# Kernel optimization log

Measured on AMD Instinct MI355X. Metric: run time of the kernel, lower is better.

## Reference

```python
import jax, jax.numpy as jnp
import numpy as np

B, C, H, W = 8, 128, 128, 128
NUM_HEADS = 4
KERNEL = 7
SH, SW = 16, 16


def setup_inputs() -> dict:
    key = jax.random.key(0)
    ks = jax.random.split(key, 5)
    s = 0.02
    return {
        "x": jax.random.normal(ks[0], (B, C, H, W), jnp.float32),
        "sims": jax.random.uniform(ks[1], (B, H, W, SH, SW), jnp.float32),
        "qk_w": jax.random.normal(ks[2], (2 * C, C), jnp.float32) * s,
        "v_w": jax.random.normal(ks[3], (C, C), jnp.float32) * s,
        "proj_w": jax.random.normal(ks[4], (C, C), jnp.float32) * s,
    }


def _nbr_starts(n, k):
    # NATTEN border handling: window start clamped so every query sees k neighbors
    return jnp.clip(jnp.arange(n) - k // 2, 0, n - k)


def reference(x, sims, qk_w, v_w, proj_w):
    Bb, Cc, Hh, Ww = x.shape
    hd = Cc // NUM_HEADS
    scale = hd ** -0.5
    xp = jnp.transpose(x, (0, 2, 3, 1))                       # [B,H,W,C]

    qk = xp @ qk_w.T                                           # [B,H,W,2C]
    q = (qk[..., :Cc]).reshape(Bb, Hh, Ww, NUM_HEADS, hd) * scale
    k = (qk[..., Cc:]).reshape(Bb, Hh, Ww, NUM_HEADS, hd)
    v = (xp @ v_w.T).reshape(Bb, Hh, Ww, NUM_HEADS, hd)

    sh_start = _nbr_starts(Hh, KERNEL)                         # [H]
    sw_start = _nbr_starts(Ww, KERNEL)                         # [W]

    # get_indices: nearest-interp superpixel grid label per pixel
    si = (jnp.arange(Hh) * SH) // Hh
    sj = (jnp.arange(Ww) * SW) // Ww
    slabel = si[:, None] * SW + sj[None, :]                    # [H,W]
    # hard superpixel assignment (argmax of sims); one_hot(argmax) gather
    # over sinds == equality test against the label map
    L = jnp.argmax(sims.reshape(Bb, Hh, Ww, SH * SW), axis=-1) # [B,H,W]

    attn_l, pi_l = [], []
    for di in range(KERNEL):
        hh = sh_start + di
        for dj in range(KERNEL):
            ww = sw_start + dj
            kk = k[:, hh][:, :, ww]                            # [B,H,W,h,d]
            attn_l.append(jnp.einsum('bijhd,bijhd->bhij', q, kk))
            pi_l.append((L[:, hh][:, :, ww] == slabel[None]).astype(x.dtype))
    attn = jnp.stack(attn_l, axis=-1)                          # [B,h,H,W,K2]
    pi = jnp.stack(pi_l, axis=-1)                              # [B,H,W,K2]

    # superpixel-masked softmax: softmax over window, reweight by membership
    # of neighbor in query's superpixel, renormalize
    p = jax.nn.softmax(attn, axis=-1) * pi[:, None]
    p = p / (jnp.sum(p, axis=-1, keepdims=True) + 1e-8)

    out = jnp.zeros_like(v)
    idx = 0
    for di in range(KERNEL):
        hh = sh_start + di
        for dj in range(KERNEL):
            ww = sw_start + dj
            vv = v[:, hh][:, :, ww]                            # [B,H,W,h,d]
            out = out + jnp.einsum('bhij,bijhd->bijhd', p[..., idx], vv)
            idx += 1

    out = out.reshape(Bb, Hh, Ww, Cc) @ proj_w.T               # proj
    return jnp.transpose(out, (0, 3, 1, 2))                    # [B,C,H,W]
```

## Files before the change

### kernel.cpp

```cpp
#include <hip/hip_runtime.h>
#include <hip/hip_bf16.h>

#define CCH 128
#define HHH 128
#define WWW 128
#define HWX 16384
#define NHD 4
#define HD  32
#define SCALE 0.17677669529663687f
#define LOG2E 1.4426950408889634f

typedef unsigned int  u32;
typedef unsigned short u16;
typedef short s16x8 __attribute__((ext_vector_type(8)));
typedef float f32x4 __attribute__((ext_vector_type(4)));

__device__ __forceinline__ u16 f2bf(float f) {
  u32 u = __float_as_uint(f);
  u += 0x7fffu + ((u >> 16) & 1u);
  return (u16)(u >> 16);
}
__device__ __forceinline__ u32 pk2(float a, float b) {
  return (u32)f2bf(a) | ((u32)f2bf(b) << 16);
}
__device__ __forceinline__ u32 pkru(float a, float b) {
  u32 ua = __float_as_uint(a) + 0x8000u;
  u32 ub = __float_as_uint(b) + 0x8000u;
  return __builtin_amdgcn_perm(ub, ua, 0x07060302);
}

__global__ __launch_bounds__(256) void wtrans_kernel(
    const float* __restrict__ qk_w, const float* __restrict__ v_w,
    const float* __restrict__ proj_w, u16* __restrict__ wfq, u16* __restrict__ wfp) {
  int idx = blockIdx.x * 256 + threadIdx.x;
  if (idx < 49152) {
    int j = idx & 7, l = (idx >> 3) & 63, kk = (idx >> 9) & 3, nt = idx >> 11;
    int k = kk * 32 + (l >> 4) * 8 + j;
    int oc = nt * 16 + (l & 15);
    float val;
    if (oc < 256) { val = qk_w[oc * 128 + k]; if (oc < 128) val *= SCALE * LOG2E; }
    else          { val = v_w[(oc - 256) * 128 + k]; }
    wfq[idx] = f2bf(val);
  } else {
    int r = idx - 49152;
    int j = r & 7, l = (r >> 3) & 63, kk = (r >> 9) & 3, mt = r >> 11;
    int oc = mt * 16 + (l & 15);
    int k = kk * 32 + (l >> 4) * 8 + j;
    wfp[r] = f2bf(proj_w[oc * 128 + k]);
  }
}

__global__ __launch_bounds__(256) void argmax_kernel(
    const float* __restrict__ sims, int* __restrict__ L) {
  const int wave = threadIdx.x >> 6, lane = threadIdx.x & 63;
  const int pix = blockIdx.x * 4 + wave;
  const float4 s4 = *(const float4*)(sims + (size_t)pix * 256 + lane * 4);
  float bv = s4.x; int bi = lane * 4;
  if (s4.y > bv) { bv = s4.y; bi = lane * 4 + 1; }
  if (s4.z > bv) { bv = s4.z; bi = lane * 4 + 2; }
  if (s4.w > bv) { bv = s4.w; bi = lane * 4 + 3; }
  #pragma unroll
  for (int off = 32; off > 0; off >>= 1) {
    float ov = __shfl_down(bv, off);
    int   oi = __shfl_down(bi, off);
    if (ov > bv || (ov == bv && oi < bi)) { bv = ov; bi = oi; }
  }
  if (lane == 0) L[pix] = bi;
}

__global__ __launch_bounds__(256) void qkv_kernel(
    const float* __restrict__ x, const u16* __restrict__ wfq,
    u16* __restrict__ qb, u16* __restrict__ kb, u16* __restrict__ vb) {
  __shared__ __align__(16) u16 xs[64 * 136];
  const int t = threadIdx.x;
  const int pg0 = blockIdx.x * 64;
  const int b = blockIdx.x >> 8;
  const int hw0 = pg0 & (HWX - 1);
  const float* xb = x + (size_t)b * (CCH * HWX) + hw0;
  u32* xsw = (u32*)xs;
  #pragma unroll
  for (int it = 0; it < 16; ++it) {
    int flat = t + it * 256;
    int pix = flat & 63, c2 = flat >> 6;
    float f0 = xb[(size_t)(2 * c2) * HWX + pix];
    float f1 = xb[(size_t)(2 * c2 + 1) * HWX + pix];
    xsw[pix * 68 + c2] = pk2(f0, f1);
  }
  __syncthreads();

  const int w = t >> 6, lane = t & 63;
  const int l15 = lane & 15, quad = lane >> 4;

  s16x8 af[4][4];
  #pragma unroll
  for (int m = 0; m < 4; ++m)
    #pragma unroll
    for (int kk = 0; kk < 4; ++kk)
      af[m][kk] = *(const s16x8*)(xs + (m * 16 + l15) * 136 + kk * 32 + quad * 8);

  f32x4 acc[6][4];
  #pragma unroll
  for (int nt = 0; nt < 6; ++nt)
    #pragma unroll
    for (int m = 0; m < 4; ++m) acc[nt][m] = (f32x4){0.f, 0.f, 0.f, 0.f};

  const u16* wl = wfq + lane * 8;
  #pragma unroll
  for (int nt = 0; nt < 6; ++nt) {
    const int ntg = w * 6 + nt;
    s16x8 bf[4];
    #pragma unroll
    for (int kk = 0; kk < 4; ++kk)
      bf[kk] = *(const s16x8*)(wl + (size_t)(ntg * 4 + kk) * 512);
    #pragma unroll
    for (int m = 0; m < 4; ++m)
      #pragma unroll
      for (int kk = 0; kk < 4; ++kk)
        acc[nt][m] = __builtin_amdgcn_mfma_f32_16x16x32_bf16(af[m][kk], bf[kk], acc[nt][m], 0, 0, 0);
  }

  #pragma unroll
  for (int nt = 0; nt < 6; ++nt) {
    const int oc = (w * 6 + nt) * 16 + l15;
    u16* base; int off;
    if (oc < 128)      { base = qb; off = oc; }
    else if (oc < 256) { base = kb; off = oc - 128; }
    else               { base = vb; off = oc - 256; }
    #pragma unroll
    for (int m = 0; m < 4; ++m) {
      const int pr = pg0 + m * 16 + quad * 4;
      #pragma unroll
      for (int r = 0; r < 4; ++r)
        base[((size_t)(pr + r) << 7) + off] = f2bf(acc[nt][m][r]);
    }
  }
}

#define VROW 520
#define PROW 72
__global__ __launch_bounds__(256, 2) void attn_kernel(
    const u16* __restrict__ qb, const u16* __restrict__ kb, const u16* __restrict__ vb,
    const int* __restrict__ L, u16* __restrict__ aob) {
  __shared__ __align__(16) u16 vT[32 * VROW];
  __shared__ __align__(16) u16 pT[256 * PROW];
  __shared__ __align__(16) u32 meta[512];
  const int t = threadIdx.x;
  const int bid = blockIdx.x;
  const int h = bid & 3, tj = (bid >> 2) & 7, ti = (bid >> 5) & 7, b = bid >> 8;
  const int i0 = ti * 16, j0 = tj * 16;
  const int r0 = i0 - 3, c0 = j0 - 3;
  const size_t bbase = (size_t)b * HWX;

  #pragma unroll
  for (int it = 0; it < 8; ++it) {
    int flat = t + it * 256;
    int key = flat >> 2, dq = flat & 3;
    int kr = key / 22, kc = key - kr * 22;
    int pr = min(max(r0 + kr, 0), HHH - 1), pc = min(max(c0 + kc, 0), WWW - 1);
    size_t g = ((bbase + (size_t)pr * WWW + pc) << 7) + h * HD + dq * 8;
    uint4 vv = *(const uint4*)(vb + g);
    u16* cb = vT + key + (size_t)(dq * 8) * VROW;
    cb[0 * VROW] = (u16)vv.x; cb[1 * VROW] = (u16)(vv.x >> 16);
    cb[2 * VROW] = (u16)vv.y; cb[3 * VROW] = (u16)(vv.y >> 16);
    cb[4 * VROW] = (u16)vv.z; cb[5 * VROW] = (u16)(vv.z >> 16);
    cb[6 * VROW] = (u16)vv.w; cb[7 * VROW] = (u16)(vv.w >> 16);
  }
  #pragma unroll
  for (int it = 0; it < 2; ++it) {
    int key = t + it * 256;
    int kr = key / 22, kc = key - kr * 22;
    int pr = min(max(r0 + kr, 0), HHH - 1), pc = min(max(c0 + kc, 0), WWW - 1);
    int lab = L[bbase + (size_t)pr * WWW + pc];
    u32 rm = 0;
    #pragma unroll
    for (int nt = 0; nt < 16; ++nt) {
      int rs = min(max(i0 + nt - 3, 0), HHH - 7) - r0;
      rm |= (u32)((u32)(kr - rs) <= 6u) << nt;
    }
    meta[key] = (u32)lab | ((u32)kc << 8) | (rm << 16);
  }
  __syncthreads();

  const int w = t >> 6, lane = t & 63;
  const int l15 = lane & 15, quad = lane >> 4;
  const int qj = j0 + l15;
  const u32 cs_rel = (u32)(min(max(qj - 3, 0), WWW - 7) - c0);
  const int ntg0 = w * 4;

  u32 slab[4];
  s16x8 qf[4];
  #pragma unroll
  for (int nt = 0; nt < 4; ++nt) {
    int qi = i0 + ntg0 + nt;
    slab[nt] = (u32)(((qi >> 3) << 4) | (qj >> 3));
    qf[nt] = *(const s16x8*)(qb + ((bbase + (size_t)qi * WWW + qj) << 7) + h * HD + quad * 8);
  }
  const int qrow0 = (ntg0 * 16 + l15) * PROW;

  f32x4 o[2][4];
  #pragma unroll
  for (int dmt = 0; dmt < 2; ++dmt)
    #pragma unroll
    for (int nt = 0; nt < 4; ++nt) o[dmt][nt] = (f32x4){0.f, 0.f, 0.f, 0.f};
  float sa[4] = {0.f, 0.f, 0.f, 0.f}, sm[4] = {0.f, 0.f, 0.f, 0.f};

  auto kaddr = [&](int key) -> const u16* {
    int kr = key / 22, kc = key - kr * 22;
    int pr = min(max(r0 + kr, 0), HHH - 1), pc = min(max(c0 + kc, 0), WWW - 1);
    return kb + ((bbase + (size_t)pr * WWW + pc) << 7) + h * HD + quad * 8;
  };

  s16x8 kf_cur = *(const s16x8*)kaddr(l15);
  s16x8 kf_nxt = *(const s16x8*)kaddr(16 + l15);

  for (int ch = 0; ch < 8; ++ch) {
    #pragma unroll
    for (int mt = 0; mt < 4; ++mt) {
      const s16x8 kf_pre = *(const s16x8*)kaddr(min(ch * 64 + mt * 16 + 32 + l15, 511));
      f32x4 s0 = __builtin_amdgcn_mfma_f32_16x16x32_bf16(kf_cur, qf[0], (f32x4){0.f,0.f,0.f,0.f}, 0, 0, 0);
      f32x4 s1 = __builtin_amdgcn_mfma_f32_16x16x32_bf16(kf_cur, qf[1], (f32x4){0.f,0.f,0.f,0.f}, 0, 0, 0);
      f32x4 s2 = __builtin_amdgcn_mfma_f32_16x16x32_bf16(kf_cur, qf[2], (f32x4){0.f,0.f,0.f,0.f}, 0, 0, 0);
      f32x4 s3 = __builtin_amdgcn_mfma_f32_16x16x32_bf16(kf_cur, qf[3], (f32x4){0.f,0.f,0.f,0.f}, 0, 0, 0);
      kf_cur = kf_nxt; kf_nxt = kf_pre;

      const uint4 me4 = *(const uint4*)(meta + ch * 64 + mt * 16 + quad * 4);
      u32 winc[4], lab[4], rm[4];
      { const u32 me[4] = {me4.x, me4.y, me4.z, me4.w};
        #pragma unroll
        for (int r = 0; r < 4; ++r) {
          winc[r] = (u32)(((me[r] >> 8) & 31u) - cs_rel <= 6u);
          lab[r]  = me[r] & 0xFFu;
          rm[r]   = me[r] >> (16 + ntg0);
        } }
      #pragma unroll
      for (int nt = 0; nt < 4; ++nt) {
        const f32x4 s_ = (nt == 0) ? s0 : (nt == 1) ? s1 : (nt == 2) ? s2 : s3;
        float pv[4];
        #pragma unroll
        for (int r = 0; r < 4; ++r) {
          const u32 win = winc[r] & ((rm[r] >> nt) & 1u);
          const u32 mem = win & (u32)(lab[r] == slab[nt]);
          const float e = __builtin_amdgcn_exp2f(s_[r]);
          sa[nt] += win ? e : 0.f;
          const float p = mem ? e : 0.f;
          sm[nt] += p;
          pv[r] = p;
        }
        *(uint2*)(pT + qrow0 + nt * 16 * PROW + mt * 16 + quad * 4) =
            make_uint2(pkru(pv[0], pv[1]), pkru(pv[2], pv[3]));
      }
    }
    #pragma unroll
    for (int kk = 0; kk < 2; ++kk) {
      s16x8 pf[4];
      #pragma unroll
      for (int nt = 0; nt < 4; ++nt)
        pf[nt] = *(const s16x8*)(pT + qrow0 + nt * 16 * PROW + kk * 32 + quad * 8);
      #pragma unroll
      for (int dmt = 0; dmt < 2; ++dmt) {
        const s16x8 vf = *(const s16x8*)(vT + (size_t)(dmt * 16 + l15) * VROW + ch * 64 + kk * 32 + quad * 8);
        #pragma unroll
        for (int nt = 0; nt < 4; ++nt)
          o[dmt][nt] = __builtin_amdgcn_mfma_f32_16x16x32_bf16(vf, pf[nt], o[dmt][nt], 0, 0, 0);
      }
    }
  }

  #pragma unroll
  for (int nt = 0; nt < 4; ++nt) {
    float a = sa[nt], m = sm[nt];
    a += __shfl_xor(a, 16); a += __shfl_xor(a, 32);
    m += __shfl_xor(m, 16); m += __shfl_xor(m, 32);
    const float inv = 1.f / (m + 1e-8f * a);
    const size_t pix = bbase + (size_t)(i0 + ntg0 + nt) * WWW + qj;
    u16* op = aob + (pix << 7) + h * HD + quad * 4;
    #pragma unroll
    for (int dmt = 0; dmt < 2; ++dmt) {
      f32x4 oo = o[dmt][nt];
      *(uint2*)(op + dmt * 16) = make_uint2(pk2(oo[0] * inv, oo[1] * inv),
                                            pk2(oo[2] * inv, oo[3] * inv));
    }
  }
}

__global__ __launch_bounds__(256) void proj_kernel(
    const u16* __restrict__ aob, const u16* __restrict__ wfp, float* __restrict__ out) {
  __shared__ __align__(16) u16 as_[64 * 136];
  const int t = threadIdx.x;
  const int pg0 = blockIdx.x * 64;
  const int b = blockIdx.x >> 8;
  const int hw0 = pg0 & (HWX - 1);
  #pragma unroll
  for (int it = 0; it < 4; ++it) {
    int flat = t + it * 256;
    int pix = flat >> 4, k8 = flat & 15;
    uint4 v = *(const uint4*)(aob + ((size_t)(pg0 + pix) << 7) + k8 * 8);
    *(uint4*)(as_ + pix * 136 + k8 * 8) = v;
  }
  __syncthreads();

  const int w = t >> 6, lane = t & 63;
  const int l15 = lane & 15, quad = lane >> 4;

  s16x8 aw[2][4];
  const u16* wl = wfp + lane * 8;
  #pragma unroll
  for (int mt = 0; mt < 2; ++mt)
    #pragma unroll
    for (int kk = 0; kk < 4; ++kk)
      aw[mt][kk] = *(const s16x8*)(wl + (size_t)((2 * w + mt) * 4 + kk) * 512);

  f32x4 acc[2][4];
  #pragma unroll
  for (int mt = 0; mt < 2; ++mt)
    #pragma unroll
    for (int nt = 0; nt < 4; ++nt) acc[mt][nt] = (f32x4){0.f, 0.f, 0.f, 0.f};

  #pragma unroll
  for (int nt = 0; nt < 4; ++nt) {
    s16x8 bf[4];
    #pragma unroll
    for (int kk = 0; kk < 4; ++kk)
      bf[kk] = *(const s16x8*)(as_ + (nt * 16 + l15) * 136 + kk * 32 + quad * 8);
    #pragma unroll
    for (int mt = 0; mt < 2; ++mt)
      #pragma unroll
      for (int kk = 0; kk < 4; ++kk)
        acc[mt][nt] = __builtin_amdgcn_mfma_f32_16x16x32_bf16(aw[mt][kk], bf[kk], acc[mt][nt], 0, 0, 0);
  }

  float* ob = out + (size_t)b * (CCH * HWX) + hw0;
  #pragma unroll
  for (int mt = 0; mt < 2; ++mt) {
    const int oc0 = (2 * w + mt) * 16 + quad * 4;
    #pragma unroll
    for (int nt = 0; nt < 4; ++nt) {
      const int pix = nt * 16 + l15;
      #pragma unroll
      for (int r = 0; r < 4; ++r)
        ob[(size_t)(oc0 + r) * HWX + pix] = acc[mt][nt][r];
    }
  }
}

extern "C" void kernel_launch(void* const* d_in, const int* in_sizes, int n_in,
                              void* d_out, int out_size, void* d_ws, size_t ws_size,
                              hipStream_t stream) {
  const float* x      = (const float*)d_in[0];
  const float* sims   = (const float*)d_in[1];
  const float* qk_w   = (const float*)d_in[2];
  const float* v_w    = (const float*)d_in[3];
  const float* proj_w = (const float*)d_in[4];
  float* out = (float*)d_out;

  u16* qb  = (u16*)d_ws;
  u16* kb  = qb + 16777216;
  u16* vb  = kb + 16777216;
  u16* aob = vb + 16777216;
  int* L   = (int*)(aob + 16777216);
  u16* wfq = (u16*)(L + 131072);
  u16* wfp = wfq + 49152;

  wtrans_kernel<<<256, 256, 0, stream>>>(qk_w, v_w, proj_w, wfq, wfp);
  argmax_kernel<<<32768, 256, 0, stream>>>(sims, L);
  qkv_kernel<<<2048, 256, 0, stream>>>(x, wfq, qb, kb, vb);
  attn_kernel<<<2048, 256, 0, stream>>>(qb, kb, vb, L, aob);
  proj_kernel<<<2048, 256, 0, stream>>>(aob, wfp, out);
}
```

Measured before the change: 409.1 us.

## Skip out-of-window key tiles in attention and stage QKV outputs via LDS

```diff
diff --git a/kernel.cpp b/kernel.cpp
--- a/kernel.cpp
+++ b/kernel.cpp
@@ -28,6 +28,7 @@
   u32 ub = __float_as_uint(b) + 0x8000u;
   return __builtin_amdgcn_perm(ub, ua, 0x07060302);
 }
+__device__ __forceinline__ int d22(int k) { return (k * 2980) >> 16; }
 
 __global__ __launch_bounds__(256) void wtrans_kernel(
     const float* __restrict__ qk_w, const float* __restrict__ v_w,
@@ -68,16 +69,17 @@
   if (lane == 0) L[pix] = bi;
 }
 
+#define XTROW 392
 __global__ __launch_bounds__(256) void qkv_kernel(
     const float* __restrict__ x, const u16* __restrict__ wfq,
     u16* __restrict__ qb, u16* __restrict__ kb, u16* __restrict__ vb) {
-  __shared__ __align__(16) u16 xs[64 * 136];
+  __shared__ __align__(16) union { u16 xs[64 * 136]; u16 xt[64 * XTROW]; } sm;
   const int t = threadIdx.x;
   const int pg0 = blockIdx.x * 64;
   const int b = blockIdx.x >> 8;
   const int hw0 = pg0 & (HWX - 1);
   const float* xb = x + (size_t)b * (CCH * HWX) + hw0;
-  u32* xsw = (u32*)xs;
+  u32* xsw = (u32*)sm.xs;
   #pragma unroll
   for (int it = 0; it < 16; ++it) {
     int flat = t + it * 256;
@@ -88,7 +90,8 @@
   }
   __syncthreads();
 
-  const int w = t >> 6, lane = t & 63;
+  const int wu = __builtin_amdgcn_readfirstlane(t >> 6);
+  const int lane = t & 63;
   const int l15 = lane & 15, quad = lane >> 4;
 
   s16x8 af[4][4];
@@ -96,42 +99,39 @@
   for (int m = 0; m < 4; ++m)
     #pragma unroll
     for (int kk = 0; kk < 4; ++kk)
-      af[m][kk] = *(const s16x8*)(xs + (m * 16 + l15) * 136 + kk * 32 + quad * 8);
-
-  f32x4 acc[6][4];
-  #pragma unroll
-  for (int nt = 0; nt < 6; ++nt)
-    #pragma unroll
-    for (int m = 0; m < 4; ++m) acc[nt][m] = (f32x4){0.f, 0.f, 0.f, 0.f};
+      af[m][kk] = *(const s16x8*)(sm.xs + (m * 16 + l15) * 136 + kk * 32 + quad * 8);
+  __syncthreads();
 
   const u16* wl = wfq + lane * 8;
   #pragma unroll
   for (int nt = 0; nt < 6; ++nt) {
-    const int ntg = w * 6 + nt;
+    const int ntg = wu * 6 + nt;
     s16x8 bf[4];
     #pragma unroll
     for (int kk = 0; kk < 4; ++kk)
       bf[kk] = *(const s16x8*)(wl + (size_t)(ntg * 4 + kk) * 512);
     #pragma unroll
-    for (int m = 0; m < 4; ++m)
+    for (int m = 0; m < 4; ++m) {
+      f32x4 acc = (f32x4){0.f, 0.f, 0.f, 0.f};
       #pragma unroll
       for (int kk = 0; kk < 4; ++kk)
-        acc[nt][m] = __builtin_amdgcn_mfma_f32_16x16x32_bf16(af[m][kk], bf[kk], acc[nt][m], 0, 0, 0);
-  }
-
-  #pragma unroll
-  for (int nt = 0; nt < 6; ++nt) {
-    const int oc = (w * 6 + nt) * 16 + l15;
-    u16* base; int off;
-    if (oc < 128)      { base = qb; off = oc; }
-    else if (oc < 256) { base = kb; off = oc - 128; }
-    else               { base = vb; off = oc - 256; }
-    #pragma unroll
-    for (int m = 0; m < 4; ++m) {
-      const int pr = pg0 + m * 16 + quad * 4;
-      #pragma unroll
-      for (int r = 0; r < 4; ++r)
-        base[((size_t)(pr + r) << 7) + off] = f2bf(acc[nt][m][r]);
+        acc = __builtin_amdgcn_mfma_f32_16x16x32_bf16(bf[kk], af[m][kk], acc, 0, 0, 0);
+      *(uint2*)(sm.xt + (m * 16 + l15) * XTROW + ntg * 16 + quad * 4) =
+          make_uint2(pk2(acc[0], acc[1]), pk2(acc[2], acc[3]));
+    }
+  }
+  __syncthreads();
+
+  u16* bufs[3] = {qb, kb, vb};
+  #pragma unroll
+  for (int bsel = 0; bsel < 3; ++bsel) {
+    u16* dst = bufs[bsel];
+    #pragma unroll
+    for (int it = 0; it < 4; ++it) {
+      int flat = t + it * 256;
+      int pix = flat >> 4, g8 = flat & 15;
+      *(uint4*)(dst + ((size_t)(pg0 + pix) << 7) + g8 * 8) =
+          *(const uint4*)(sm.xt + pix * XTROW + bsel * 128 + g8 * 8);
     }
   }
 }
@@ -144,6 +144,7 @@
   __shared__ __align__(16) u16 vT[32 * VROW];
   __shared__ __align__(16) u16 pT[256 * PROW];
   __shared__ __align__(16) u32 meta[512];
+  __shared__ __align__(16) u32 koff[512];
   const int t = threadIdx.x;
   const int bid = blockIdx.x;
   const int h = bid & 3, tj = (bid >> 2) & 7, ti = (bid >> 5) & 7, b = bid >> 8;
@@ -155,7 +156,7 @@
   for (int it = 0; it < 8; ++it) {
     int flat = t + it * 256;
     int key = flat >> 2, dq = flat & 3;
-    int kr = key / 22, kc = key - kr * 22;
+    int kr = d22(key), kc = key - kr * 22;
     int pr = min(max(r0 + kr, 0), HHH - 1), pc = min(max(c0 + kc, 0), WWW - 1);
     size_t g = ((bbase + (size_t)pr * WWW + pc) << 7) + h * HD + dq * 8;
     uint4 vv = *(const uint4*)(vb + g);
@@ -168,8 +169,9 @@
   #pragma unroll
   for (int it = 0; it < 2; ++it) {
     int key = t + it * 256;
-    int kr = key / 22, kc = key - kr * 22;
+    int kr = d22(key), kc = key - kr * 22;
     int pr = min(max(r0 + kr, 0), HHH - 1), pc = min(max(c0 + kc, 0), WWW - 1);
+    koff[key] = (u32)(pr * WWW + pc);
     int lab = L[bbase + (size_t)pr * WWW + pc];
     u32 rm = 0;
     #pragma unroll
@@ -181,17 +183,20 @@
   }
   __syncthreads();
 
-  const int w = t >> 6, lane = t & 63;
+  const int wu = __builtin_amdgcn_readfirstlane(t >> 6);
+  const int lane = t & 63;
   const int l15 = lane & 15, quad = lane >> 4;
   const int qj = j0 + l15;
   const u32 cs_rel = (u32)(min(max(qj - 3, 0), WWW - 7) - c0);
-  const int ntg0 = w * 4;
-
+  const int ntg0 = wu * 4;
+
+  int rsr[4];
   u32 slab[4];
   s16x8 qf[4];
   #pragma unroll
   for (int nt = 0; nt < 4; ++nt) {
     int qi = i0 + ntg0 + nt;
+    rsr[nt] = min(max(qi - 3, 0), HHH - 7) - r0;
     slab[nt] = (u32)(((qi >> 3) << 4) | (qj >> 3));
     qf[nt] = *(const s16x8*)(qb + ((bbase + (size_t)qi * WWW + qj) << 7) + h * HD + quad * 8);
   }
@@ -204,64 +209,74 @@
     for (int nt = 0; nt < 4; ++nt) o[dmt][nt] = (f32x4){0.f, 0.f, 0.f, 0.f};
   float sa[4] = {0.f, 0.f, 0.f, 0.f}, sm[4] = {0.f, 0.f, 0.f, 0.f};
 
-  auto kaddr = [&](int key) -> const u16* {
-    int kr = key / 22, kc = key - kr * 22;
-    int pr = min(max(r0 + kr, 0), HHH - 1), pc = min(max(c0 + kc, 0), WWW - 1);
-    return kb + ((bbase + (size_t)pr * WWW + pc) << 7) + h * HD + quad * 8;
+  auto kaddr = [&](int tile) -> const u16* {
+    u32 vo = koff[tile + l15];
+    return kb + ((bbase + vo) << 7) + h * HD + quad * 8;
   };
 
-  s16x8 kf_cur = *(const s16x8*)kaddr(l15);
-  s16x8 kf_nxt = *(const s16x8*)kaddr(16 + l15);
+  s16x8 kf_cur = *(const s16x8*)kaddr(0);
+  s16x8 kf_nxt = *(const s16x8*)kaddr(16);
 
   for (int ch = 0; ch < 8; ++ch) {
     #pragma unroll
     for (int mt = 0; mt < 4; ++mt) {
-      const s16x8 kf_pre = *(const s16x8*)kaddr(min(ch * 64 + mt * 16 + 32 + l15, 511));
-      f32x4 s0 = __builtin_amdgcn_mfma_f32_16x16x32_bf16(kf_cur, qf[0], (f32x4){0.f,0.f,0.f,0.f}, 0, 0, 0);
-      f32x4 s1 = __builtin_amdgcn_mfma_f32_16x16x32_bf16(kf_cur, qf[1], (f32x4){0.f,0.f,0.f,0.f}, 0, 0, 0);
-      f32x4 s2 = __builtin_amdgcn_mfma_f32_16x16x32_bf16(kf_cur, qf[2], (f32x4){0.f,0.f,0.f,0.f}, 0, 0, 0);
-      f32x4 s3 = __builtin_amdgcn_mfma_f32_16x16x32_bf16(kf_cur, qf[3], (f32x4){0.f,0.f,0.f,0.f}, 0, 0, 0);
-      kf_cur = kf_nxt; kf_nxt = kf_pre;
-
-      const uint4 me4 = *(const uint4*)(meta + ch * 64 + mt * 16 + quad * 4);
-      u32 winc[4], lab[4], rm[4];
-      { const u32 me[4] = {me4.x, me4.y, me4.z, me4.w};
+      const int k0 = ch * 64 + mt * 16;
+      const s16x8 kf_pre = *(const s16x8*)kaddr(min(k0 + 32, 496));
+      const int rlo = d22(k0), rhi = d22(k0 + 15);
+      if (rlo <= rsr[3] + 6 && rhi >= rsr[0]) {
+        const uint4 me4 = *(const uint4*)(meta + k0 + quad * 4);
+        u32 winc[4], lab[4], rm[4];
+        { const u32 me[4] = {me4.x, me4.y, me4.z, me4.w};
+          #pragma unroll
+          for (int r = 0; r < 4; ++r) {
+            winc[r] = (u32)(((me[r] >> 8) & 31u) - cs_rel <= 6u);
+            lab[r]  = me[r] & 0xFFu;
+            rm[r]   = me[r] >> (16 + ntg0);
+          } }
         #pragma unroll
-        for (int r = 0; r < 4; ++r) {
-          winc[r] = (u32)(((me[r] >> 8) & 31u) - cs_rel <= 6u);
-          lab[r]  = me[r] & 0xFFu;
-          rm[r]   = me[r] >> (16 + ntg0);
-        } }
-      #pragma unroll
-      for (int nt = 0; nt < 4; ++nt) {
-        const f32x4 s_ = (nt == 0) ? s0 : (nt == 1) ? s1 : (nt == 2) ? s2 : s3;
-        float pv[4];
-        #pragma unroll
-        for (int r = 0; r < 4; ++r) {
-          const u32 win = winc[r] & ((rm[r] >> nt) & 1u);
-          const u32 mem = win & (u32)(lab[r] == slab[nt]);
-          const float e = __builtin_amdgcn_exp2f(s_[r]);
-          sa[nt] += win ? e : 0.f;
-          const float p = mem ? e : 0.f;
-          sm[nt] += p;
-          pv[r] = p;
+        for (int nt = 0; nt < 4; ++nt) {
+          if (rlo <= rsr[nt] + 6 && rhi >= rsr[nt]) {
+            const f32x4 s_ = __builtin_amdgcn_mfma_f32_16x16x32_bf16(
+                kf_cur, qf[nt], (f32x4){0.f, 0.f, 0.f, 0.f}, 0, 0, 0);
+            float pv[4];
+            #pragma unroll
+            for (int r = 0; r < 4; ++r) {
+              const u32 win = winc[r] & ((rm[r] >> nt) & 1u);
+              const u32 mem = win & (u32)(lab[r] == slab[nt]);
+              const float e = __builtin_amdgcn_exp2f(s_[r]);
+              sa[nt] += win ? e : 0.f;
+              const float p = mem ? e : 0.f;
+              sm[nt] += p;
+              pv[r] = p;
+            }
+            *(uint2*)(pT + qrow0 + nt * 16 * PROW + mt * 16 + quad * 4) =
+                make_uint2(pkru(pv[0], pv[1]), pkru(pv[2], pv[3]));
+          } else {
+            *(uint2*)(pT + qrow0 + nt * 16 * PROW + mt * 16 + quad * 4) = make_uint2(0u, 0u);
+          }
         }
-        *(uint2*)(pT + qrow0 + nt * 16 * PROW + mt * 16 + quad * 4) =
-            make_uint2(pkru(pv[0], pv[1]), pkru(pv[2], pv[3]));
-      }
-    }
-    #pragma unroll
-    for (int kk = 0; kk < 2; ++kk) {
-      s16x8 pf[4];
-      #pragma unroll
-      for (int nt = 0; nt < 4; ++nt)
-        pf[nt] = *(const s16x8*)(pT + qrow0 + nt * 16 * PROW + kk * 32 + quad * 8);
-      #pragma unroll
-      for (int dmt = 0; dmt < 2; ++dmt) {
-        const s16x8 vf = *(const s16x8*)(vT + (size_t)(dmt * 16 + l15) * VROW + ch * 64 + kk * 32 + quad * 8);
+      } else {
         #pragma unroll
         for (int nt = 0; nt < 4; ++nt)
-          o[dmt][nt] = __builtin_amdgcn_mfma_f32_16x16x32_bf16(vf, pf[nt], o[dmt][nt], 0, 0, 0);
+          *(uint2*)(pT + qrow0 + nt * 16 * PROW + mt * 16 + quad * 4) = make_uint2(0u, 0u);
+      }
+      kf_cur = kf_nxt; kf_nxt = kf_pre;
+    }
+    #pragma unroll
+    for (int kk = 0; kk < 2; ++kk) {
+      const int kb0 = ch * 64 + kk * 32;
+      const int r2lo = d22(kb0), r2hi = d22(kb0 + 31);
+      if (r2lo <= rsr[3] + 6 && r2hi >= rsr[0]) {
+        const s16x8 vf0 = *(const s16x8*)(vT + (size_t)l15 * VROW + kb0 + quad * 8);
+        const s16x8 vf1 = *(const s16x8*)(vT + (size_t)(16 + l15) * VROW + kb0 + quad * 8);
+        #pragma unroll
+        for (int nt = 0; nt < 4; ++nt) {
+          if (r2lo <= rsr[nt] + 6 && r2hi >= rsr[nt]) {
+            const s16x8 pf = *(const s16x8*)(pT + qrow0 + nt * 16 * PROW + kk * 32 + quad * 8);
+            o[0][nt] = __builtin_amdgcn_mfma_f32_16x16x32_bf16(vf0, pf, o[0][nt], 0, 0, 0);
+            o[1][nt] = __builtin_amdgcn_mfma_f32_16x16x32_bf16(vf1, pf, o[1][nt], 0, 0, 0);
+          }
+        }
       }
     }
   }
```

Result: faster. 364.5 us (-10.9%).
